# Kernel tuning notes

Measured on AMD Instinct MI355X. Metric: run time of the kernel, lower is better.

## Reference

```python
import jax, jax.numpy as jnp
import numpy as np

NX = 4096
NY = 4096
DX = 0.01
DY = 0.01
DT = 0.001
CX = 1.0
CY = 1.0
CXW = DT / DX / 2.0 * CX  # 0.05, x-direction stencil coefficient
CYW = DT / DY / 2.0 * CY  # 0.05, y-direction stencil coefficient
DIAG = 1.0                # A[1,1]
NLEVEL = int(np.log2(min(NX, NY))) + 1  # 13


def _smooth(x):
    # 3x3 cross-correlation with kernel A, valid padding (stride 1, no pad).
    # A[0,1]=CYW, A[2,1]=-CYW, A[1,0]=CXW, A[1,1]=1, A[1,2]=-CXW.
    return (CYW * x[:-2, 1:-1] - CYW * x[2:, 1:-1]
            + CXW * x[1:-1, :-2] + x[1:-1, 1:-1] - CXW * x[1:-1, 2:])


def _bc(u):
    # Replicate edges (not corners: corners stay exactly 0, as in the torch code).
    H, W = u.shape
    p = jnp.zeros((H + 2, W + 2), u.dtype)
    p = p.at[1:-1, 1:-1].set(u)
    p = p.at[0, 1:-1].set(u[0])
    p = p.at[-1, 1:-1].set(u[-1])
    p = p.at[1:-1, 0].set(u[:, 0])
    p = p.at[1:-1, -1].set(u[:, -1])
    return p


def _restrict(x):
    # 2x2 average pooling, stride 2 (conv weight = 0.25 everywhere).
    return 0.25 * (x[0::2, 0::2] + x[1::2, 0::2] + x[0::2, 1::2] + x[1::2, 1::2])


def _prolong(x):
    # Nearest-neighbor upsample by 2.
    return jnp.repeat(jnp.repeat(x, 2, axis=0), 2, axis=1)


def setup_inputs() -> dict:
    key = jax.random.key(0)
    u = jax.random.normal(key, (1, 1, NY, NX), dtype=jnp.float32)
    return {"u": u, "t": 4}


def reference(u, t):
    v = u[0, 0]  # (NY, NX)
    for _ in range(t):  # t outer F-cycle iterations (b = 0 source term)
        r = _smooth(_bc(v))  # residual on finest grid, (NY, NX)
        r_s = [r]
        for _i in range(1, NLEVEL - 3):
            r = _restrict(r)
            r_s.append(r)  # coarsest stored level is 8x8
        e = jnp.zeros((1, 1), v.dtype)
        for j in reversed(range(1, NLEVEL - 3)):
            # coarse-grid correction; broadcast of (small e) + r_s[j] matches torch
            e = e - _smooth(jnp.pad(e, 1)) / DIAG + r_s[j] / DIAG
            e = _prolong(e)
        v = v - e
        v = v - _smooth(_bc(v)) / DIAG
    return v[None, None]
```

## Files before the change

### kernel.cpp

```cpp
#include <hip/hip_runtime.h>
#include <cstddef>


constexpr float CW = 0.05f;

__device__ __forceinline__ float up_val(float Pc, float Pu, float Pd, float Pl,
                                        float Pr, float rv) {
  float sm = CW * Pu - CW * Pd + CW * Pl + Pc - CW * Pr;
  return (Pc - sm) + rv;
}

__device__ __forceinline__ float e1_at(const float* __restrict__ E2,
                                       const float* __restrict__ r1,
                                       int a, int b) {
  const int h = 2048, s2 = 1024;
  float Pc = E2[(size_t)(a >> 1) * s2 + (b >> 1)];
  float Pu = (a > 0)     ? E2[(size_t)((a - 1) >> 1) * s2 + (b >> 1)] : 0.0f;
  float Pd = (a < h - 1) ? E2[(size_t)((a + 1) >> 1) * s2 + (b >> 1)] : 0.0f;
  float Pl = (b > 0)     ? E2[(size_t)(a >> 1) * s2 + ((b - 1) >> 1)] : 0.0f;
  float Pr = (b < h - 1) ? E2[(size_t)(a >> 1) * s2 + ((b + 1) >> 1)] : 0.0f;
  return up_val(Pc, Pu, Pd, Pl, Pr, r1[(size_t)a * h + b]);
}

__global__ __launch_bounds__(256) void k_sr_chain(
    const float* __restrict__ v, float* __restrict__ r1,
    float* __restrict__ r2, float* __restrict__ r3,
    float* __restrict__ r4, float* __restrict__ r5) {
  const int n = 4096, h = 2048;
  __shared__ float r1s[64][65];
  __shared__ float r2s[32][33];
  __shared__ float r3s[16][17];
  __shared__ float r4s[8][9];
  int tid = threadIdx.x;
  int bx = blockIdx.x, by = blockIdx.y;
  int ty0 = by * 64, tx0 = bx * 64;

#pragma unroll
  for (int k = 0; k < 4; ++k) {
    int u = tid + 256 * k;
    int uy = u >> 5, ux = u & 31;
    int bi = (ty0 >> 1) + uy;
    int bj = (tx0 >> 1) + ux;
    int c0 = 4 * bj;
    int cl = max(c0 - 1, 0), cr = min(c0 + 4, n - 1);
    float a[6][6];
#pragma unroll
    for (int rr = 0; rr < 6; ++rr) {
      int R = min(max(4 * bi - 1 + rr, 0), n - 1);
      const float* row = v + (size_t)R * n;
      float4 m = *reinterpret_cast<const float4*>(row + c0);
      a[rr][0] = row[cl];
      a[rr][1] = m.x; a[rr][2] = m.y; a[rr][3] = m.z; a[rr][4] = m.w;
      a[rr][5] = row[cr];
    }
#pragma unroll
    for (int oi = 0; oi < 2; ++oi) {
      float2 o;
#pragma unroll
      for (int oj = 0; oj < 2; ++oj) {
        float s[2][2];
#pragma unroll
        for (int p = 0; p < 2; ++p)
#pragma unroll
          for (int q = 0; q < 2; ++q) {
            int P = 2 * oi + p, Q = 2 * oj + q;
            s[p][q] = CW * a[P][Q + 1] - CW * a[P + 2][Q + 1]
                    + CW * a[P + 1][Q] + a[P + 1][Q + 1] - CW * a[P + 1][Q + 2];
          }
        float val = 0.25f * (((s[0][0] + s[1][0]) + s[0][1]) + s[1][1]);
        (oj ? o.y : o.x) = val;
        r1s[2 * uy + oi][2 * ux + oj] = val;
      }
      *reinterpret_cast<float2*>(r1 + (size_t)(2 * bi + oi) * h + 2 * bj) = o;
    }
  }
  __syncthreads();

#pragma unroll
  for (int k = 0; k < 4; ++k) {
    int idx = tid + 256 * k;
    int I = idx >> 5, J = idx & 31;
    float val = 0.25f * (((r1s[2 * I][2 * J] + r1s[2 * I + 1][2 * J])
                          + r1s[2 * I][2 * J + 1]) + r1s[2 * I + 1][2 * J + 1]);
    r2s[I][J] = val;
    r2[(size_t)(32 * by + I) * 1024 + 32 * bx + J] = val;
  }
  __syncthreads();

  {
    int I = tid >> 4, J = tid & 15;
    float val = 0.25f * (((r2s[2 * I][2 * J] + r2s[2 * I + 1][2 * J])
                          + r2s[2 * I][2 * J + 1]) + r2s[2 * I + 1][2 * J + 1]);
    r3s[I][J] = val;
    r3[(size_t)(16 * by + I) * 512 + 16 * bx + J] = val;
  }
  __syncthreads();

  if (tid < 64) {
    int I = tid >> 3, J = tid & 7;
    float val = 0.25f * (((r3s[2 * I][2 * J] + r3s[2 * I + 1][2 * J])
                          + r3s[2 * I][2 * J + 1]) + r3s[2 * I + 1][2 * J + 1]);
    r4s[I][J] = val;
    r4[(size_t)(8 * by + I) * 256 + 8 * bx + J] = val;
  }
  __syncthreads();

  if (tid < 16) {
    int I = tid >> 2, J = tid & 3;
    float val = 0.25f * (((r4s[2 * I][2 * J] + r4s[2 * I + 1][2 * J])
                          + r4s[2 * I][2 * J + 1]) + r4s[2 * I + 1][2 * J + 1]);
    r5[(size_t)(4 * by + I) * 128 + 4 * bx + J] = val;
  }
}

__global__ __launch_bounds__(256, 1) void k_mid(
    const float* __restrict__ r5, const float* __restrict__ r4,
    const float* __restrict__ r3, const float* __restrict__ r2,
    float* __restrict__ E2) {
  __shared__ float r5s[128 * 128];
  __shared__ float r6s[64 * 64];
  __shared__ float r7s[32 * 32];
  __shared__ float r8s[16 * 16];
  __shared__ float r9s[8 * 8];
  __shared__ float E8s[16 * 16];
  __shared__ float E7s[32 * 32];
  __shared__ float E6s[64 * 64];
  __shared__ float e5r[10][128];
  __shared__ float e4s[18][20];
  __shared__ float e3s[34][35];
  int tid = threadIdx.x;
  int bx = blockIdx.x, by = blockIdx.y;

  auto up_lds = [&](const float* Ep, const float* rr, int i, int c, int nn) {
    int ss = nn >> 1;
    float Pc = Ep[(i >> 1) * ss + (c >> 1)];
    float Pu = (i > 0)      ? Ep[((i - 1) >> 1) * ss + (c >> 1)] : 0.0f;
    float Pd = (i < nn - 1) ? Ep[((i + 1) >> 1) * ss + (c >> 1)] : 0.0f;
    float Pl = (c > 0)      ? Ep[(i >> 1) * ss + ((c - 1) >> 1)] : 0.0f;
    float Pr = (c < nn - 1) ? Ep[(i >> 1) * ss + ((c + 1) >> 1)] : 0.0f;
    return up_val(Pc, Pu, Pd, Pl, Pr, rr[i * nn + c]);
  };

  for (int idx = tid; idx < 4096; idx += 256)
    reinterpret_cast<float4*>(r5s)[idx] = reinterpret_cast<const float4*>(r5)[idx];
  __syncthreads();
  for (int idx = tid; idx < 64 * 64; idx += 256) {
    int I = idx >> 6, J = idx & 63;
    float a = r5s[(2 * I) * 128 + 2 * J],     b = r5s[(2 * I + 1) * 128 + 2 * J];
    float c = r5s[(2 * I) * 128 + 2 * J + 1], d = r5s[(2 * I + 1) * 128 + 2 * J + 1];
    r6s[idx] = 0.25f * (((a + b) + c) + d);
  }
  __syncthreads();
  for (int idx = tid; idx < 32 * 32; idx += 256) {
    int I = idx >> 5, J = idx & 31;
    float a = r6s[(2 * I) * 64 + 2 * J],     b = r6s[(2 * I + 1) * 64 + 2 * J];
    float c = r6s[(2 * I) * 64 + 2 * J + 1], d = r6s[(2 * I + 1) * 64 + 2 * J + 1];
    r7s[idx] = 0.25f * (((a + b) + c) + d);
  }
  __syncthreads();
  if (tid < 16 * 16) {
    int I = tid >> 4, J = tid & 15;
    float a = r7s[(2 * I) * 32 + 2 * J],     b = r7s[(2 * I + 1) * 32 + 2 * J];
    float c = r7s[(2 * I) * 32 + 2 * J + 1], d = r7s[(2 * I + 1) * 32 + 2 * J + 1];
    r8s[tid] = 0.25f * (((a + b) + c) + d);
  }
  __syncthreads();
  if (tid < 8 * 8) {
    int I = tid >> 3, J = tid & 7;
    float a = r8s[(2 * I) * 16 + 2 * J],     b = r8s[(2 * I + 1) * 16 + 2 * J];
    float c = r8s[(2 * I) * 16 + 2 * J + 1], d = r8s[(2 * I + 1) * 16 + 2 * J + 1];
    r9s[tid] = 0.25f * (((a + b) + c) + d);
  }
  __syncthreads();
  if (tid < 16 * 16)
    E8s[tid] = up_lds(r9s, r8s, tid >> 4, tid & 15, 16);
  __syncthreads();
  if (tid < 32 * 32)
    E7s[tid] = up_lds(E8s, r7s, tid >> 5, tid & 31, 32);
  __syncthreads();
  for (int idx = tid; idx < 64 * 64; idx += 256)
    E6s[idx] = up_lds(E7s, r6s, idx >> 6, idx & 63, 64);
  __syncthreads();
  for (int idx = tid; idx < 10 * 128; idx += 256) {
    int t = idx >> 7, c = idx & 127;
    int i = min(max(8 * by - 1 + t, 0), 127);
    e5r[t][c] = up_lds(E6s, r5s, i, c, 128);
  }
  __syncthreads();
  for (int idx = tid; idx < 18 * 18; idx += 256) {
    int er = idx / 18, ec = idx % 18;
    int ga = 16 * by - 1 + er, gb = 16 * bx - 1 + ec;
    if (ga >= 0 && ga < 256 && gb >= 0 && gb < 256) {
      float Pc = e5r[(ga >> 1) - (8 * by - 1)][gb >> 1];
      float Pu = (ga > 0)   ? e5r[((ga - 1) >> 1) - (8 * by - 1)][gb >> 1] : 0.0f;
      float Pd = (ga < 255) ? e5r[((ga + 1) >> 1) - (8 * by - 1)][gb >> 1] : 0.0f;
      float Pl = (gb > 0)   ? e5r[(ga >> 1) - (8 * by - 1)][(gb - 1) >> 1] : 0.0f;
      float Pr = (gb < 255) ? e5r[(ga >> 1) - (8 * by - 1)][(gb + 1) >> 1] : 0.0f;
      e4s[er][ec] = up_val(Pc, Pu, Pd, Pl, Pr, r4[(size_t)ga * 256 + gb]);
    }
  }
  __syncthreads();
  for (int idx = tid; idx < 34 * 34; idx += 256) {
    int er = idx / 34, ec = idx % 34;
    int gr = 32 * by - 1 + er, gc = 32 * bx - 1 + ec;
    float val = 0.0f;
    if (gr >= 0 && gr < 512 && gc >= 0 && gc < 512) {
      int e4r0 = 16 * by - 1, e4c0 = 16 * bx - 1;
      float Pc = e4s[(gr >> 1) - e4r0][(gc >> 1) - e4c0];
      float Pu = (gr > 0)   ? e4s[((gr - 1) >> 1) - e4r0][(gc >> 1) - e4c0] : 0.0f;
      float Pd = (gr < 511) ? e4s[((gr + 1) >> 1) - e4r0][(gc >> 1) - e4c0] : 0.0f;
      float Pl = (gc > 0)   ? e4s[(gr >> 1) - e4r0][((gc - 1) >> 1) - e4c0] : 0.0f;
      float Pr = (gc < 511) ? e4s[(gr >> 1) - e4r0][((gc + 1) >> 1) - e4c0] : 0.0f;
      val = up_val(Pc, Pu, Pd, Pl, Pr, r3[(size_t)gr * 512 + gc]);
    }
    e3s[er][ec] = val;
  }
  __syncthreads();
  int br0 = 32 * by - 1, bc0 = 32 * bx - 1;
#pragma unroll
  for (int k = 0; k < 4; ++k) {
    int u = tid + 256 * k;
    int rr = u >> 4, f = u & 15;
    int gR = 64 * by + rr;
    int gC = 64 * bx + 4 * f;
    int rc = (gR >> 1) - br0;
    int ru = ((gR - 1) >> 1) - br0;
    int rd = ((gR + 1) >> 1) - br0;
    float4 rv = *reinterpret_cast<const float4*>(r2 + (size_t)gR * 1024 + gC);
    float4 o;
#pragma unroll
    for (int q = 0; q < 4; ++q) {
      int c = gC + q;
      int lc = (c >> 1) - bc0;
      float Pc = e3s[rc][lc];
      float Pu = (gR > 0)    ? e3s[ru][lc] : 0.0f;
      float Pd = (gR < 1023) ? e3s[rd][lc] : 0.0f;
      float Pl = (c > 0)     ? e3s[rc][((c - 1) >> 1) - bc0] : 0.0f;
      float Pr = (c < 1023)  ? e3s[rc][((c + 1) >> 1) - bc0] : 0.0f;
      (&o.x)[q] = up_val(Pc, Pu, Pd, Pl, Pr, (&rv.x)[q]);
    }
    *reinterpret_cast<float4*>(E2 + (size_t)gR * 1024 + gC) = o;
  }
}

__global__ __launch_bounds__(256) void k_final(
    const float* __restrict__ v, const float* __restrict__ E2,
    const float* __restrict__ r1, float* __restrict__ out) {
  const int n = 4096;
  int J = blockIdx.x * blockDim.x + threadIdx.x;
  int i = blockIdx.y * blockDim.y + threadIdx.y;
  int c0 = 4 * J;
  int cl = max(c0 - 1, 0), cr = min(c0 + 4, n - 1);
  int ecl = cl >> 1, ecr = cr >> 1;

  float e[3][4];
  int ers0 = max(2 * i - 1, 0) >> 1;
  int ers2 = min(2 * i + 2, n - 1) >> 1;
  const int ers[3] = {ers0, i, ers2};
#pragma unroll
  for (int t = 0; t < 3; ++t) {
    int a = ers[t];
    e[t][0] = e1_at(E2, r1, a, ecl);
    e[t][1] = e1_at(E2, r1, a, 2 * J);
    e[t][2] = e1_at(E2, r1, a, 2 * J + 1);
    e[t][3] = e1_at(E2, r1, a, ecr);
  }

  float w[4][6];
  const int tmap[4] = {0, 1, 1, 2};
#pragma unroll
  for (int rr = 0; rr < 4; ++rr) {
    int R = min(max(2 * i - 1 + rr, 0), n - 1);
    int t = tmap[rr];
    const float* vrow = v + (size_t)R * n;
    float4 m = *reinterpret_cast<const float4*>(vrow + c0);
    w[rr][0] = vrow[cl] - e[t][0];
    w[rr][1] = m.x - e[t][1];
    w[rr][2] = m.y - e[t][1];
    w[rr][3] = m.z - e[t][2];
    w[rr][4] = m.w - e[t][2];
    w[rr][5] = vrow[cr] - e[t][3];
  }
#pragma unroll
  for (int a = 0; a < 2; ++a) {
    float4 o;
#pragma unroll
    for (int qq = 0; qq < 4; ++qq) {
      float ce = w[a + 1][qq + 1];
      float sm = CW * w[a][qq + 1] - CW * w[a + 2][qq + 1]
               + CW * w[a + 1][qq] + ce - CW * w[a + 1][qq + 2];
      (&o.x)[qq] = ce - sm;
    }
    *reinterpret_cast<float4*>(out + (size_t)(2 * i + a) * n + c0) = o;
  }
}

extern "C" void kernel_launch(void* const* d_in, const int* in_sizes, int n_in,
                              void* d_out, int out_size, void* d_ws, size_t ws_size,
                              hipStream_t stream) {
  (void)in_sizes; (void)n_in; (void)out_size;
  float* u = (float*)d_in[0];
  float* out = (float*)d_out;
  char* ws = (char*)d_ws;

  size_t off = 0;
  auto alloc = [&](size_t elems) {
    float* p = (float*)(ws + off);
    off += (elems * sizeof(float) + 255) & ~(size_t)255;
    return p;
  };
  float* r1 = alloc(2048 * 2048);
  float* r2 = alloc(1024 * 1024);
  float* r3 = alloc(512 * 512);
  float* r4 = alloc(256 * 256);
  float* r5 = alloc(128 * 128);
  float* E2 = alloc(1024 * 1024);
  size_t pool = off;
  const size_t VB = (size_t)4096 * 4096 * sizeof(float);
  bool big = ws_size >= pool + VB;
  float* vws = (float*)(ws + pool);

  auto iterate = [&](const float* vin, float* vout) {
    k_sr_chain<<<dim3(32, 32), 256, 0, stream>>>(vin, r1, r2, r3, r4, r5);
    k_mid<<<dim3(16, 16), 256, 0, stream>>>(r5, r4, r3, r2, E2);
    k_final<<<dim3(16, 512), dim3(64, 4), 0, stream>>>(vin, E2, r1, vout);
  };

  if (big) {
    iterate(u, vws);
    iterate(vws, out);
    iterate(out, vws);
    iterate(vws, out);
  } else {
    iterate(u, out);
    iterate(out, u);
    iterate(u, out);
    iterate(out, u);
    hipMemcpyAsync(out, u, VB, hipMemcpyDeviceToDevice, stream);
  }
}
```

Before: 455.8 us.

## Materialize finest-level correction in separate kernel and widen residual tiles per thread

Adds a k_up kernel that computes the 2048x2048 correction E1 once from E2 and r1, so k_final reads precomputed values instead of recomputing the 5-point upsample stencil for each of its 12 e-samples per thread. k_sr_chain is also restructured so each thread computes a 4x4 tile of r1 with a sliding row window of v, reusing loaded rows across output rows instead of reloading overlapping halos. The cost is an extra launch and a 16 MB write plus read of E1 per iteration, and higher register use in k_sr_chain.

```diff
diff --git a/kernel.cpp b/kernel.cpp
--- a/kernel.cpp
+++ b/kernel.cpp
@@ -8,18 +8,6 @@
                                         float Pr, float rv) {
   float sm = CW * Pu - CW * Pd + CW * Pl + Pc - CW * Pr;
   return (Pc - sm) + rv;
-}
-
-__device__ __forceinline__ float e1_at(const float* __restrict__ E2,
-                                       const float* __restrict__ r1,
-                                       int a, int b) {
-  const int h = 2048, s2 = 1024;
-  float Pc = E2[(size_t)(a >> 1) * s2 + (b >> 1)];
-  float Pu = (a > 0)     ? E2[(size_t)((a - 1) >> 1) * s2 + (b >> 1)] : 0.0f;
-  float Pd = (a < h - 1) ? E2[(size_t)((a + 1) >> 1) * s2 + (b >> 1)] : 0.0f;
-  float Pl = (b > 0)     ? E2[(size_t)(a >> 1) * s2 + ((b - 1) >> 1)] : 0.0f;
-  float Pr = (b < h - 1) ? E2[(size_t)(a >> 1) * s2 + ((b + 1) >> 1)] : 0.0f;
-  return up_val(Pc, Pu, Pd, Pl, Pr, r1[(size_t)a * h + b]);
 }
 
 __global__ __launch_bounds__(256) void k_sr_chain(
@@ -32,46 +20,52 @@
   __shared__ float r3s[16][17];
   __shared__ float r4s[8][9];
   int tid = threadIdx.x;
+  int tx = tid & 15, ty = tid >> 4;
   int bx = blockIdx.x, by = blockIdx.y;
-  int ty0 = by * 64, tx0 = bx * 64;
-
-#pragma unroll
-  for (int k = 0; k < 4; ++k) {
-    int u = tid + 256 * k;
-    int uy = u >> 5, ux = u & 31;
-    int bi = (ty0 >> 1) + uy;
-    int bj = (tx0 >> 1) + ux;
-    int c0 = 4 * bj;
-    int cl = max(c0 - 1, 0), cr = min(c0 + 4, n - 1);
-    float a[6][6];
-#pragma unroll
-    for (int rr = 0; rr < 6; ++rr) {
-      int R = min(max(4 * bi - 1 + rr, 0), n - 1);
-      const float* row = v + (size_t)R * n;
-      float4 m = *reinterpret_cast<const float4*>(row + c0);
-      a[rr][0] = row[cl];
-      a[rr][1] = m.x; a[rr][2] = m.y; a[rr][3] = m.z; a[rr][4] = m.w;
-      a[rr][5] = row[cr];
-    }
-#pragma unroll
-    for (int oi = 0; oi < 2; ++oi) {
-      float2 o;
-#pragma unroll
-      for (int oj = 0; oj < 2; ++oj) {
-        float s[2][2];
-#pragma unroll
-        for (int p = 0; p < 2; ++p)
-#pragma unroll
-          for (int q = 0; q < 2; ++q) {
-            int P = 2 * oi + p, Q = 2 * oj + q;
-            s[p][q] = CW * a[P][Q + 1] - CW * a[P + 2][Q + 1]
-                    + CW * a[P + 1][Q] + a[P + 1][Q + 1] - CW * a[P + 1][Q + 2];
-          }
-        float val = 0.25f * (((s[0][0] + s[1][0]) + s[0][1]) + s[1][1]);
-        (oj ? o.y : o.x) = val;
-        r1s[2 * uy + oi][2 * ux + oj] = val;
-      }
-      *reinterpret_cast<float2*>(r1 + (size_t)(2 * bi + oi) * h + 2 * bj) = o;
+  int g0 = 64 * by + 4 * ty;
+  int h0 = 64 * bx + 4 * tx;
+  int C0 = 2 * h0;
+  int cl = max(C0 - 1, 0), cr = min(C0 + 8, n - 1);
+
+  float va[4][10];
+  auto loadrow = [&](int R, float* dst) {
+    R = min(max(R, 0), n - 1);
+    const float* row = v + (size_t)R * n;
+    float4 m0 = *reinterpret_cast<const float4*>(row + C0);
+    float4 m1 = *reinterpret_cast<const float4*>(row + C0 + 4);
+    dst[0] = row[cl];
+    dst[1] = m0.x; dst[2] = m0.y; dst[3] = m0.z; dst[4] = m0.w;
+    dst[5] = m1.x; dst[6] = m1.y; dst[7] = m1.z; dst[8] = m1.w;
+    dst[9] = row[cr];
+  };
+#pragma unroll
+  for (int r = 0; r < 4; ++r) loadrow(2 * g0 - 1 + r, va[r]);
+
+#pragma unroll
+  for (int rr = 0; rr < 4; ++rr) {
+    int g = g0 + rr;
+    float4 o;
+#pragma unroll
+    for (int cc = 0; cc < 4; ++cc) {
+      float s[2][2];
+#pragma unroll
+      for (int p = 0; p < 2; ++p)
+#pragma unroll
+        for (int q = 0; q < 2; ++q) {
+          s[p][q] = CW * va[p][2 * cc + 1 + q] - CW * va[p + 2][2 * cc + 1 + q]
+                  + CW * va[p + 1][2 * cc + q] + va[p + 1][2 * cc + 1 + q]
+                  - CW * va[p + 1][2 * cc + 2 + q];
+        }
+      float val = 0.25f * (((s[0][0] + s[1][0]) + s[0][1]) + s[1][1]);
+      (&o.x)[cc] = val;
+      r1s[4 * ty + rr][4 * tx + cc] = val;
+    }
+    *reinterpret_cast<float4*>(r1 + (size_t)g * h + h0) = o;
+    if (rr < 3) {
+#pragma unroll
+      for (int c = 0; c < 10; ++c) { va[0][c] = va[2][c]; va[1][c] = va[3][c]; }
+      loadrow(2 * g + 3, va[2]);
+      loadrow(2 * g + 4, va[3]);
     }
   }
   __syncthreads();
@@ -86,7 +80,6 @@
     r2[(size_t)(32 * by + I) * 1024 + 32 * bx + J] = val;
   }
   __syncthreads();
-
   {
     int I = tid >> 4, J = tid & 15;
     float val = 0.25f * (((r2s[2 * I][2 * J] + r2s[2 * I + 1][2 * J])
@@ -95,7 +88,6 @@
     r3[(size_t)(16 * by + I) * 512 + 16 * bx + J] = val;
   }
   __syncthreads();
-
   if (tid < 64) {
     int I = tid >> 3, J = tid & 7;
     float val = 0.25f * (((r3s[2 * I][2 * J] + r3s[2 * I + 1][2 * J])
@@ -104,7 +96,6 @@
     r4[(size_t)(8 * by + I) * 256 + 8 * bx + J] = val;
   }
   __syncthreads();
-
   if (tid < 16) {
     int I = tid >> 2, J = tid & 3;
     float val = 0.25f * (((r4s[2 * I][2 * J] + r4s[2 * I + 1][2 * J])
@@ -243,10 +234,44 @@
   }
 }
 
+__global__ __launch_bounds__(256) void k_up(
+    const float* __restrict__ Ep, const float* __restrict__ r,
+    float* __restrict__ Eo, int n) {
+  int s = n >> 1;
+  int j = blockIdx.x * blockDim.x + threadIdx.x;
+  int i = blockIdx.y * blockDim.y + threadIdx.y;
+  if (i >= s || j >= (n >> 2)) return;
+  const float* ec = Ep + (size_t)i * s + 2 * j;
+  float epc0 = ec[0], epc1 = ec[1];
+  float epl = (j > 0) ? ec[-1] : 0.0f;
+  float epr = (2 * j + 2 < s) ? ec[2] : 0.0f;
+  float epu0 = 0.0f, epu1 = 0.0f, epd0 = 0.0f, epd1 = 0.0f;
+  if (i > 0)     { epu0 = ec[-s]; epu1 = ec[-s + 1]; }
+  if (i < s - 1) { epd0 = ec[s];  epd1 = ec[s + 1]; }
+  {
+    float4 rv = *reinterpret_cast<const float4*>(r + (size_t)(2 * i) * n + 4 * j);
+    float4 o;
+    o.x = up_val(epc0, epu0, epc0, epl,  epc0, rv.x);
+    o.y = up_val(epc0, epu0, epc0, epc0, epc1, rv.y);
+    o.z = up_val(epc1, epu1, epc1, epc0, epc1, rv.z);
+    o.w = up_val(epc1, epu1, epc1, epc1, epr,  rv.w);
+    *reinterpret_cast<float4*>(Eo + (size_t)(2 * i) * n + 4 * j) = o;
+  }
+  {
+    float4 rv = *reinterpret_cast<const float4*>(r + (size_t)(2 * i + 1) * n + 4 * j);
+    float4 o;
+    o.x = up_val(epc0, epc0, epd0, epl,  epc0, rv.x);
+    o.y = up_val(epc0, epc0, epd0, epc0, epc1, rv.y);
+    o.z = up_val(epc1, epc1, epd1, epc0, epc1, rv.z);
+    o.w = up_val(epc1, epc1, epd1, epc1, epr,  rv.w);
+    *reinterpret_cast<float4*>(Eo + (size_t)(2 * i + 1) * n + 4 * j) = o;
+  }
+}
+
 __global__ __launch_bounds__(256) void k_final(
-    const float* __restrict__ v, const float* __restrict__ E2,
-    const float* __restrict__ r1, float* __restrict__ out) {
-  const int n = 4096;
+    const float* __restrict__ v, const float* __restrict__ E1,
+    float* __restrict__ out) {
+  const int n = 4096, h = 2048;
   int J = blockIdx.x * blockDim.x + threadIdx.x;
   int i = blockIdx.y * blockDim.y + threadIdx.y;
   int c0 = 4 * J;
@@ -259,11 +284,11 @@
   const int ers[3] = {ers0, i, ers2};
 #pragma unroll
   for (int t = 0; t < 3; ++t) {
-    int a = ers[t];
-    e[t][0] = e1_at(E2, r1, a, ecl);
-    e[t][1] = e1_at(E2, r1, a, 2 * J);
-    e[t][2] = e1_at(E2, r1, a, 2 * J + 1);
-    e[t][3] = e1_at(E2, r1, a, ecr);
+    const float* erow = E1 + (size_t)ers[t] * h;
+    e[t][0] = erow[ecl];
+    e[t][1] = erow[2 * J];
+    e[t][2] = erow[2 * J + 1];
+    e[t][3] = erow[ecr];
   }
 
   float w[4][6];
@@ -315,15 +340,18 @@
   float* r4 = alloc(256 * 256);
   float* r5 = alloc(128 * 128);
   float* E2 = alloc(1024 * 1024);
+  float* E1 = alloc(2048 * 2048);
   size_t pool = off;
   const size_t VB = (size_t)4096 * 4096 * sizeof(float);
   bool big = ws_size >= pool + VB;
   float* vws = (float*)(ws + pool);
 
+  dim3 b(64, 4);
   auto iterate = [&](const float* vin, float* vout) {
     k_sr_chain<<<dim3(32, 32), 256, 0, stream>>>(vin, r1, r2, r3, r4, r5);
     k_mid<<<dim3(16, 16), 256, 0, stream>>>(r5, r4, r3, r2, E2);
-    k_final<<<dim3(16, 512), dim3(64, 4), 0, stream>>>(vin, E2, r1, vout);
+    k_up<<<dim3(8, 256), b, 0, stream>>>(E2, r1, E1, 2048);
+    k_final<<<dim3(16, 512), b, 0, stream>>>(vin, E1, vout);
   };
 
   if (big) {
```

After: 397.9 us. -12.7%, faster.
